# Performance work log

Hardware: AMD Instinct MI355X
Metric: run time of the kernel (lower is better)

The kernel has to match this reference:

```python
import jax, jax.numpy as jnp
import numpy as np

B, N, C = 1, 32768, 256
NH, F, AG, P = 8, 32, 64, 4  # heads, cube side, agent tokens, pool size (P**3==AG)
HD = C // NH


def setup_inputs() -> dict:
    key = jax.random.key(0)
    ks = jax.random.split(key, 4)
    s = 0.02
    return {
        "x": jax.random.normal(ks[0], (B, N, C), jnp.float32),
        "w_qkv": jax.random.normal(ks[1], (3 * C, C), jnp.float32) * s,
        "b_qkv": jnp.zeros((3 * C,), jnp.float32),
        "w_proj": jax.random.normal(ks[2], (C, C), jnp.float32) * s,
        "b_proj": jnp.zeros((C,), jnp.float32),
        "w_dwc": jax.random.normal(ks[3], (C, C, 3, 3, 3), jnp.float32) * s,
        "b_dwc": jnp.zeros((C,), jnp.float32),
    }


def reference(x, w_qkv, b_qkv, w_proj, b_proj, w_dwc, b_dwc):
    scale = HD ** -0.5
    # qkv projection -> (3, B*NH, N, HD), replicating torch reshape/permute exactly
    qkv = x @ w_qkv.T + b_qkv                       # (B, N, 3C)
    qkv = qkv.reshape(B, N, 3, NH, HD)
    qkv = jnp.transpose(qkv, (2, 0, 3, 1, 4)).reshape(3, B * NH, N, HD)
    q, k, v = qkv[0], qkv[1], qkv[2]

    # agent tokens: pool q (note torch's raw reshape interleaves heads into channels)
    q_vol = q.reshape(B, F, F, F, C)                # faithful to torch reshape
    q_vol = jnp.transpose(q_vol, (0, 4, 1, 2, 3))   # (B, C, F, F, F)
    blk = F // P
    A = q_vol.reshape(B, C, P, blk, P, blk, P, blk).mean(axis=(3, 5, 7))  # (B,C,P,P,P)
    A = A.reshape(B, C, AG).transpose(0, 2, 1)      # (B, AG, C)
    A = A.reshape(B, AG, NH, HD).transpose(0, 2, 1, 3).reshape(B * NH, AG, HD)

    # stage 1: agents attend to keys, aggregate values
    agent_attn = jax.nn.softmax((A * scale) @ jnp.swapaxes(k, -2, -1), axis=-1)  # (B*NH, AG, N)
    agent_v = agent_attn @ v                        # (B*NH, AG, HD)
    # stage 2: queries attend to agents
    q_attn = jax.nn.softmax((q * scale) @ jnp.swapaxes(A, -2, -1), axis=-1)      # (B*NH, N, AG)
    o = q_attn @ agent_v                            # (B*NH, N, HD)

    # faithful to torch: transpose(1,2) then raw reshape
    o = jnp.swapaxes(o, 1, 2).reshape(B, N, C)

    # conv residual on v: (B*NH, N, HD) -> (B, C, F, F, F)
    v5 = jnp.swapaxes(v, 1, 2).reshape(B, C, F, F, F)
    conv = jax.lax.conv_general_dilated(
        v5, w_dwc, window_strides=(1, 1, 1), padding="SAME",
        dimension_numbers=("NCDHW", "OIDHW", "NCDHW"))
    conv = conv + b_dwc[None, :, None, None, None]
    o = o + jnp.transpose(conv, (0, 2, 3, 4, 1)).reshape(B, N, C)

    return o @ w_proj.T + b_proj
```

## Files before the change

kernel.cpp:

```cpp
#include <hip/hip_runtime.h>
#include <stdint.h>

typedef unsigned short u16;
typedef __attribute__((ext_vector_type(8))) short bf16x8;
typedef __attribute__((ext_vector_type(4))) float f32x4;

#define KSCALE (0.17677669529663687f / 512.0f)

__device__ __forceinline__ u16 f2b(float f) {
  unsigned u = __float_as_uint(f);
  unsigned r = (u + 0x7fffu + ((u >> 16) & 1u)) >> 16;
  return (u16)r;
}
__device__ __forceinline__ float b2f(u16 s) { return __uint_as_float(((unsigned)s) << 16); }

__device__ __forceinline__ void async16(const void* g, void* l) {
  __builtin_amdgcn_global_load_lds((const __attribute__((address_space(1))) unsigned int*)g,
                                   (__attribute__((address_space(3))) unsigned int*)l, 16, 0, 0);
}

__device__ __forceinline__ bf16x8 frag8(const float* p, float k) {
  float4 f0 = *(const float4*)p, f1 = *(const float4*)(p + 4);
  bf16x8 v;
  v[0] = f2b(f0.x * k); v[1] = f2b(f0.y * k); v[2] = f2b(f0.z * k); v[3] = f2b(f0.w * k);
  v[4] = f2b(f1.x * k); v[5] = f2b(f1.y * k); v[6] = f2b(f1.z * k); v[7] = f2b(f1.w * k);
  return v;
}

__global__ void prep_cast(const float* __restrict__ x, const float* __restrict__ wq,
                          const float* __restrict__ wp, const float* __restrict__ wdwc,
                          u16* __restrict__ Xb, u16* __restrict__ Wqb,
                          u16* __restrict__ Wpb, u16* __restrict__ Wc) {
  int b = blockIdx.x, tid = threadIdx.x;
  if (b < 8448) {
    const float* src; u16* dst; int i;
    if (b < 8192)      { src = x;  dst = Xb;  i = b * 256 + tid; }
    else if (b < 8384) { src = wq; dst = Wqb; i = (b - 8192) * 256 + tid; }
    else               { src = wp; dst = Wpb; i = (b - 8384) * 256 + tid; }
    const float4 v = ((const float4*)src)[i];
    uint2 o;
    o.x = (unsigned)f2b(v.x) | ((unsigned)f2b(v.y) << 16);
    o.y = (unsigned)f2b(v.z) | ((unsigned)f2b(v.w) << 16);
    ((uint2*)dst)[i] = o;
  } else {
    int o = b - 8448;
    __shared__ u16 lds[6912];
    for (int t = tid; t < 6912; t += 256) lds[t] = f2b(wdwc[o * 6912 + t]);
    __syncthreads();
    for (int idx = tid; idx < 6912; idx += 256) {
      int tp = idx >> 8, i = idx & 255;
      Wc[o * 6912 + idx] = lds[i * 27 + tp];
    }
  }
}

__global__ void prep_av(const u16* __restrict__ QKV, u16* __restrict__ v5,
                        float* __restrict__ Apre) {
  int b = blockIdx.x, tid = threadIdx.x;
  if (b < 4913) {
    int idx = b * 256 + tid;
    int c8 = idx & 31, vox = idx >> 5;
    int z = vox / 1156, r2 = vox - z * 1156, y = r2 / 34, x = r2 - y * 34;
    bf16x8 val = {0, 0, 0, 0, 0, 0, 0, 0};
    if (z >= 1 && z <= 32 && y >= 1 && y <= 32 && x >= 1 && x <= 32) {
      int n = (z - 1) * 1024 + (y - 1) * 32 + (x - 1);
      val = *(const bf16x8*)(QKV + n * 768 + 512 + c8 * 8);
    }
    *(bf16x8*)(v5 + vox * 256 + c8 * 8) = val;
  } else {
    int b2 = b - 4913;
    int a = b2 >> 3, s = b2 & 7;
    int hp = tid >> 5, dp = tid & 31;
    int p1 = a >> 4, p2 = (a >> 2) & 3, p3 = a & 3;
    float sum = 0.f;
    for (int ui = 0; ui < 64; ++ui) {
      int u = s * 64 + ui;
      int f1 = p1 * 8 + (u >> 6);
      int f2 = p2 * 8 + ((u >> 3) & 7);
      int f3 = p3 * 8 + (u & 7);
      int vox = f1 * 1024 + f2 * 32 + f3;
      int n  = ((vox & 4095) << 3) + hp;
      int cq = ((vox >> 12) << 5) + dp;
      sum += b2f(QKV[n * 768 + cq]);
    }
    atomicAdd(&Apre[(hp * 64 + a) * 32 + dp], sum);
  }
}


__device__ __forceinline__ void stage64(const u16* src, int row0, int ld, int k0,
                                        short* dst, int tid) {
  int wv = tid >> 6, lane = tid & 63;
  int r15 = lane & 15, kc8 = (lane >> 4) * 8;
#pragma unroll
  for (int j = 0; j < 4; ++j) {
    int p = j & 1, g = wv * 2 + (j >> 1);
    async16(src + (row0 + g * 16 + r15) * ld + k0 + p * 32 + kc8, dst + p * 4096 + g * 512);
  }
}

__device__ __forceinline__ void mfma64(const short* As, const short* Bs, int wm, int wn,
                                       int lane, f32x4 acc[4][4]) {
  const int q = lane >> 4, c = lane & 15;
  const int fo = q * 128 + c * 8;
#pragma unroll
  for (int p = 0; p < 2; ++p) {
    bf16x8 a[4], b[4];
#pragma unroll
    for (int mt = 0; mt < 4; ++mt) a[mt] = *(const bf16x8*)&As[p * 4096 + (wm * 4 + mt) * 512 + fo];
#pragma unroll
    for (int nt = 0; nt < 4; ++nt) b[nt] = *(const bf16x8*)&Bs[p * 4096 + (wn * 4 + nt) * 512 + fo];
#pragma unroll
    for (int mt = 0; mt < 4; ++mt)
#pragma unroll
      for (int nt = 0; nt < 4; ++nt)
        acc[mt][nt] = __builtin_amdgcn_mfma_f32_16x16x32_bf16(a[mt], b[nt], acc[mt][nt], 0, 0, 0);
  }
}

__global__ __launch_bounds__(256) void gemm_qkv(const u16* __restrict__ Xb,
                                                const u16* __restrict__ Wq,
                                                const float* __restrict__ bias,
                                                u16* __restrict__ QKV) {
  const int m0 = blockIdx.x * 128, n0 = blockIdx.y * 128;
  const int tid = threadIdx.x, lane = tid & 63, wv = tid >> 6;
  const int wm = wv >> 1, wn = wv & 1, q = lane >> 4, c = lane & 15;
  __shared__ short As[8192], Bs[8192];
  f32x4 acc[4][4] = {};
  for (int kb = 0; kb < 256; kb += 64) {
    stage64(Xb, m0, 256, kb, As, tid);
    stage64(Wq, n0, 256, kb, Bs, tid);
    __syncthreads();
    mfma64(As, Bs, wm, wn, lane, acc);
    __syncthreads();
  }
#pragma unroll
  for (int nt = 0; nt < 4; ++nt) {
    int col = n0 + wn * 64 + nt * 16 + c;
    float bv = bias[col];
#pragma unroll
    for (int mt = 0; mt < 4; ++mt) {
      int row = m0 + wm * 64 + mt * 16 + q * 4;
#pragma unroll
      for (int r = 0; r < 4; ++r) QKV[(row + r) * 768 + col] = f2b(acc[mt][nt][r] + bv);
    }
  }
}

__global__ __launch_bounds__(256) void conv_s1(const u16* __restrict__ v5,
                                               const u16* __restrict__ Wc,
                                               const float* __restrict__ bias,
                                               u16* __restrict__ Xp,
                                               const u16* __restrict__ QKV,
                                               const float* __restrict__ Apre,
                                               float* __restrict__ avac,
                                               float* __restrict__ rsum) {
  extern __shared__ char smem[];
  const int tid = threadIdx.x, lane = tid & 63, wv = tid >> 6;
  const int q = lane >> 4, c = lane & 15;
  if (blockIdx.x < 512) {
    const int bid = blockIdx.x;
    const int xcd = bid & 7, idx = bid >> 3;
    const int n0 = (idx & 1) * 128;
    const int mt_i = xcd * 32 + (idx >> 1);
    const int m0 = mt_i * 128;
    const int z0 = mt_i >> 3, y0 = (mt_i & 7) * 4;
    const int wm = wv >> 1, wn = wv & 1;
    const int r15 = lane & 15, kq8 = (lane >> 4) * 8;
    short* As = (short*)smem;
    short* Bs = (short*)(smem + 9216);
    f32x4 acc[4][4] = {};
    const u16* browB = Wc + (n0 + r15) * 6912 + kq8;
    for (int dzy = 0; dzy < 9; ++dzy) {
      int dz = dzy / 3, dy = dzy - dz * 3;
      int base = (z0 + dz) * 1156 + (y0 + dy) * 34;
      int tap0 = dzy * 3;
      for (int panel = 0; panel < 8; ++panel) {
        int choff = panel * 32 + kq8;
        for (int g = wv; g < 9; g += 4) {
          int row = base + g * 16 + r15;
          row = row < 39303 ? row : 39303;
          async16(v5 + row * 256 + choff, As + g * 512);
        }
#pragma unroll
        for (int i = wv; i < 24; i += 4) {
          int dx = i >> 3, g = i & 7;
          async16(browB + g * (16 * 6912) + (tap0 + dx) * 256 + panel * 32, Bs + i * 512);
        }
        __syncthreads();
#pragma unroll
        for (int dx = 0; dx < 3; ++dx) {
          bf16x8 a[4], b[4];
#pragma unroll
          for (int mt = 0; mt < 4; ++mt) {
            int M = wm * 64 + mt * 16 + c;
            int vx = M + 2 * (M >> 5) + dx;
            a[mt] = *(const bf16x8*)&As[(vx >> 4) * 512 + q * 128 + (vx & 15) * 8];
          }
#pragma unroll
          for (int nt = 0; nt < 4; ++nt)
            b[nt] = *(const bf16x8*)&Bs[dx * 4096 + (wn * 4 + nt) * 512 + q * 128 + c * 8];
#pragma unroll
          for (int mt = 0; mt < 4; ++mt)
#pragma unroll
            for (int nt = 0; nt < 4; ++nt)
              acc[mt][nt] = __builtin_amdgcn_mfma_f32_16x16x32_bf16(a[mt], b[nt], acc[mt][nt], 0, 0, 0);
        }
        __syncthreads();
      }
    }
#pragma unroll
    for (int nt = 0; nt < 4; ++nt) {
      int col = n0 + wn * 64 + nt * 16 + c;
      float bv = bias[col];
#pragma unroll
      for (int mt = 0; mt < 4; ++mt) {
        int row = m0 + wm * 64 + mt * 16 + q * 4;
#pragma unroll
        for (int r = 0; r < 4; ++r) Xp[(row + r) * 256 + col] = f2b(acc[mt][nt][r] + bv);
      }
    }
  } else {
    const int vb = blockIdx.x - 512;
    const int h = vb >> 7, n0 = (vb & 127) * 256;
    u16* E  = (u16*)smem;
    u16* VT = (u16*)(smem + 33792);
    float* RED = (float*)smem;
    {
      const u16* vrow = QKV + (n0 + tid) * 768 + 512 + h * 32;
#pragma unroll
      for (int d8 = 0; d8 < 4; ++d8) {
        bf16x8 v = *(const bf16x8*)(vrow + d8 * 8);
#pragma unroll
        for (int e = 0; e < 8; ++e) VT[(d8 * 8 + e) * 264 + tid] = (u16)v[e];
      }
    }
    {
      bf16x8 af[4], bf[4];
#pragma unroll
      for (int mt = 0; mt < 4; ++mt)
        af[mt] = frag8(Apre + h * 2048 + (mt * 16 + c) * 32 + q * 8, KSCALE);
#pragma unroll
      for (int nt = 0; nt < 4; ++nt)
        bf[nt] = *(const bf16x8*)(QKV + (n0 + wv * 64 + nt * 16 + c) * 768 + 256 + h * 32 + q * 8);
#pragma unroll
      for (int mt = 0; mt < 4; ++mt)
#pragma unroll
        for (int nt = 0; nt < 4; ++nt) {
          f32x4 s = {0.f, 0.f, 0.f, 0.f};
          s = __builtin_amdgcn_mfma_f32_16x16x32_bf16(af[mt], bf[nt], s, 0, 0, 0);
#pragma unroll
          for (int r = 0; r < 4; ++r) {
            int a = mt * 16 + q * 4 + r, nl = wv * 64 + nt * 16 + c;
            E[a * 264 + nl] = f2b(__expf(s[r]));
          }
        }
    }
    __syncthreads();
    {
      int a = tid >> 2, seg = tid & 3;
      float sum = 0.f;
      for (int i = 0; i < 64; ++i) sum += b2f(E[a * 264 + seg * 64 + i]);
      sum += __shfl_xor(sum, 1);
      sum += __shfl_xor(sum, 2);
      if (seg == 0) atomicAdd(&rsum[h * 64 + a], sum);
    }
    f32x4 pv[4][2] = {};
#pragma unroll
    for (int ks = 0; ks < 2; ++ks) {
      bf16x8 ap[4], bp[2];
#pragma unroll
      for (int mt = 0; mt < 4; ++mt)
        ap[mt] = *(const bf16x8*)&E[(mt * 16 + c) * 264 + wv * 64 + ks * 32 + q * 8];
#pragma unroll
      for (int nt = 0; nt < 2; ++nt)
        bp[nt] = *(const bf16x8*)&VT[(nt * 16 + c) * 264 + wv * 64 + ks * 32 + q * 8];
#pragma unroll
      for (int mt = 0; mt < 4; ++mt)
#pragma unroll
        for (int nt = 0; nt < 2; ++nt)
          pv[mt][nt] = __builtin_amdgcn_mfma_f32_16x16x32_bf16(ap[mt], bp[nt], pv[mt][nt], 0, 0, 0);
    }
    __syncthreads();
#pragma unroll
    for (int mt = 0; mt < 4; ++mt)
#pragma unroll
      for (int nt = 0; nt < 2; ++nt)
#pragma unroll
        for (int r = 0; r < 4; ++r)
          RED[wv * 2048 + (mt * 16 + q * 4 + r) * 32 + nt * 16 + c] = pv[mt][nt][r];
    __syncthreads();
    for (int idx = tid; idx < 2048; idx += 256) {
      float t = RED[idx] + RED[2048 + idx] + RED[4096 + idx] + RED[6144 + idx];
      atomicAdd(&avac[h * 2048 + idx], t);
    }
  }
}

__global__ __launch_bounds__(256) void gemm_proj(const u16* __restrict__ Xp,
                                                 const u16* __restrict__ Wp,
                                                 const float* __restrict__ bias,
                                                 float* __restrict__ out) {
  const int m0 = blockIdx.x * 128, n0 = blockIdx.y * 128;
  const int tid = threadIdx.x, lane = tid & 63, wv = tid >> 6;
  const int wm = wv >> 1, wn = wv & 1, q = lane >> 4, c = lane & 15;
  __shared__ short As[8192], Bs[8192];
  f32x4 acc[4][4] = {};
  for (int kb = 0; kb < 256; kb += 64) {
    stage64(Xp, m0, 256, kb, As, tid);
    stage64(Wp, n0, 256, kb, Bs, tid);
    __syncthreads();
    mfma64(As, Bs, wm, wn, lane, acc);
    __syncthreads();
  }
#pragma unroll
  for (int nt = 0; nt < 4; ++nt) {
    int col = n0 + wn * 64 + nt * 16 + c;
    float bv = bias[col];
#pragma unroll
    for (int mt = 0; mt < 4; ++mt) {
      int row = m0 + wm * 64 + mt * 16 + q * 4;
#pragma unroll
      for (int r = 0; r < 4; ++r) out[(row + r) * 256 + col] = acc[mt][nt][r] + bv;
    }
  }
}

__global__ __launch_bounds__(256) void s2_attn(const u16* __restrict__ QKV,
                                               const float* __restrict__ Apre,
                                               const float* __restrict__ avac,
                                               const float* __restrict__ rsum,
                                               u16* __restrict__ Xp) {
  const int h = blockIdx.y, n0 = blockIdx.x * 256;
  const int tid = threadIdx.x, lane = tid & 63, wv = tid >> 6;
  const int q = lane >> 4, c = lane & 15;
  extern __shared__ char smem[];
  u16* P = (u16*)smem;
  float* O = (float*)smem;
  u16* AVT = (u16*)(smem + 36864);

  for (int j = 0; j < 8; ++j) {
    int i = j * 256 + tid;
    int a = i >> 5, d = i & 31;
    AVT[d * 72 + a] = f2b(avac[h * 2048 + i] / rsum[h * 64 + a]);
  }

  f32x4 s[4][4];
  {
    bf16x8 af[4], bf[4];
#pragma unroll
    for (int mt = 0; mt < 4; ++mt)
      af[mt] = *(const bf16x8*)(QKV + (n0 + wv * 64 + mt * 16 + c) * 768 + h * 32 + q * 8);
#pragma unroll
    for (int nt = 0; nt < 4; ++nt)
      bf[nt] = frag8(Apre + h * 2048 + (nt * 16 + c) * 32 + q * 8, KSCALE);
#pragma unroll
    for (int mt = 0; mt < 4; ++mt)
#pragma unroll
      for (int nt = 0; nt < 4; ++nt) {
        f32x4 z = {0.f, 0.f, 0.f, 0.f};
        s[mt][nt] = __builtin_amdgcn_mfma_f32_16x16x32_bf16(af[mt], bf[nt], z, 0, 0, 0);
      }
  }
#pragma unroll
  for (int mt = 0; mt < 4; ++mt)
#pragma unroll
    for (int r = 0; r < 4; ++r) {
      float v0 = s[mt][0][r], v1 = s[mt][1][r], v2 = s[mt][2][r], v3 = s[mt][3][r];
      float mx = fmaxf(fmaxf(v0, v1), fmaxf(v2, v3));
      mx = fmaxf(mx, __shfl_xor(mx, 1));
      mx = fmaxf(mx, __shfl_xor(mx, 2));
      mx = fmaxf(mx, __shfl_xor(mx, 4));
      mx = fmaxf(mx, __shfl_xor(mx, 8));
      float e0 = __expf(v0 - mx), e1 = __expf(v1 - mx), e2 = __expf(v2 - mx), e3 = __expf(v3 - mx);
      float sm = e0 + e1 + e2 + e3;
      sm += __shfl_xor(sm, 1);
      sm += __shfl_xor(sm, 2);
      sm += __shfl_xor(sm, 4);
      sm += __shfl_xor(sm, 8);
      float inv = 1.0f / sm;
      int tok = wv * 64 + mt * 16 + q * 4 + r;
      P[tok * 72 +      c] = f2b(e0 * inv);
      P[tok * 72 + 16 + c] = f2b(e1 * inv);
      P[tok * 72 + 32 + c] = f2b(e2 * inv);
      P[tok * 72 + 48 + c] = f2b(e3 * inv);
    }
  __syncthreads();
  f32x4 o[4][2] = {};
#pragma unroll
  for (int ks = 0; ks < 2; ++ks) {
    bf16x8 ap[4], bv[2];
#pragma unroll
    for (int mt = 0; mt < 4; ++mt)
      ap[mt] = *(const bf16x8*)&P[(wv * 64 + mt * 16 + c) * 72 + ks * 32 + q * 8];
#pragma unroll
    for (int nt = 0; nt < 2; ++nt)
      bv[nt] = *(const bf16x8*)&AVT[(nt * 16 + c) * 72 + ks * 32 + q * 8];
#pragma unroll
    for (int mt = 0; mt < 4; ++mt)
#pragma unroll
      for (int nt = 0; nt < 2; ++nt)
        o[mt][nt] = __builtin_amdgcn_mfma_f32_16x16x32_bf16(ap[mt], bv[nt], o[mt][nt], 0, 0, 0);
  }
  __syncthreads();
#pragma unroll
  for (int mt = 0; mt < 4; ++mt)
#pragma unroll
    for (int nt = 0; nt < 2; ++nt)
#pragma unroll
      for (int r = 0; r < 4; ++r)
        O[(nt * 16 + c) * 258 + wv * 64 + mt * 16 + q * 4 + r] = o[mt][nt][r];
  __syncthreads();
  for (int d = 0; d < 32; ++d) {
    int addr = (h * 32 + d) * 32768 + n0 + tid;
    Xp[addr] = f2b(b2f(Xp[addr]) + O[d * 258 + tid]);
  }
}


extern "C" void kernel_launch(void* const* d_in, const int* in_sizes, int n_in,
                              void* d_out, int out_size, void* d_ws, size_t ws_size,
                              hipStream_t stream) {
  const float* x      = (const float*)d_in[0];
  const float* w_qkv  = (const float*)d_in[1];
  const float* b_qkv  = (const float*)d_in[2];
  const float* w_proj = (const float*)d_in[3];
  const float* b_proj = (const float*)d_in[4];
  const float* w_dwc  = (const float*)d_in[5];
  const float* b_dwc  = (const float*)d_in[6];
  float* out = (float*)d_out;
  char* ws = (char*)d_ws;

  u16* Xb   = (u16*)(ws);
  u16* QKV  = (u16*)(ws + 16777216);
  u16* V5   = (u16*)(ws + 67108864);
  u16* Wc   = (u16*)(ws + 87232512);
  u16* Wqb  = (u16*)(ws + 90771456);
  u16* Wpb  = (u16*)(ws + 91164672);
  float* AVAC = (float*)(ws + 91361280);
  float* RSUM = (float*)(ws + 91426816);
  float* APRE = (float*)(ws + 91428864);
  u16* Xp = Xb;

  hipMemsetAsync(AVAC, 0, 65536 + 2048 + 65536, stream);
  prep_cast<<<8704, 256, 0, stream>>>(x, w_qkv, w_proj, w_dwc, Xb, Wqb, Wpb, Wc);
  gemm_qkv<<<dim3(256, 6), 256, 0, stream>>>(Xb, Wqb, b_qkv, QKV);
  prep_av<<<5425, 256, 0, stream>>>(QKV, V5, APRE);
  conv_s1<<<1536, 256, 50688, stream>>>(V5, Wc, b_dwc, Xp, QKV, APRE, AVAC, RSUM);
  s2_attn<<<dim3(128, 8), 256, 41472, stream>>>(QKV, APRE, AVAC, RSUM, Xp);
  gemm_proj<<<dim3(256, 2), 256, 0, stream>>>(Xp, Wpb, b_proj, out);
}
```

Baseline: 333.8 us.

## Halve stage-1 token tile and cut conv_s1 shared memory for higher occupancy

Stage-1 agent-attention blocks now process 128 tokens instead of 256, doubling their count to 2048. Dynamic shared memory for the fused conv/stage-1 kernel drops from 50688 to 33792 bytes, and launch bounds now request 4 blocks per CU. The cross-wave reduction is restructured into a two-phase write-then-accumulate over half the RED buffer. The goals are more resident blocks and less LDS pressure. The cost is twice as many atomicAdds into avac/rsum, and the occupancy hint may cap registers for the conv GEMM path.

```diff
diff --git a/kernel.cpp b/kernel.cpp
--- a/kernel.cpp
+++ b/kernel.cpp
@@ -147,14 +147,14 @@
   }
 }
 
-__global__ __launch_bounds__(256) void conv_s1(const u16* __restrict__ v5,
-                                               const u16* __restrict__ Wc,
-                                               const float* __restrict__ bias,
-                                               u16* __restrict__ Xp,
-                                               const u16* __restrict__ QKV,
-                                               const float* __restrict__ Apre,
-                                               float* __restrict__ avac,
-                                               float* __restrict__ rsum) {
+__global__ __launch_bounds__(256, 4) void conv_s1(const u16* __restrict__ v5,
+                                                  const u16* __restrict__ Wc,
+                                                  const float* __restrict__ bias,
+                                                  u16* __restrict__ Xp,
+                                                  const u16* __restrict__ QKV,
+                                                  const float* __restrict__ Apre,
+                                                  float* __restrict__ avac,
+                                                  float* __restrict__ rsum) {
   extern __shared__ char smem[];
   const int tid = threadIdx.x, lane = tid & 63, wv = tid >> 6;
   const int q = lane >> 4, c = lane & 15;
@@ -222,37 +222,38 @@
     }
   } else {
     const int vb = blockIdx.x - 512;
-    const int h = vb >> 7, n0 = (vb & 127) * 256;
+    const int h = vb >> 8, n0 = (vb & 255) * 128;
     u16* E  = (u16*)smem;
-    u16* VT = (u16*)(smem + 33792);
+    u16* VT = (u16*)(smem + 17408);
     float* RED = (float*)smem;
     {
-      const u16* vrow = QKV + (n0 + tid) * 768 + 512 + h * 32;
-#pragma unroll
-      for (int d8 = 0; d8 < 4; ++d8) {
+      const int tok = tid & 127, dh = (tid >> 7) * 16;
+      const u16* vrow = QKV + (n0 + tok) * 768 + 512 + h * 32 + dh;
+#pragma unroll
+      for (int d8 = 0; d8 < 2; ++d8) {
         bf16x8 v = *(const bf16x8*)(vrow + d8 * 8);
 #pragma unroll
-        for (int e = 0; e < 8; ++e) VT[(d8 * 8 + e) * 264 + tid] = (u16)v[e];
+        for (int e = 0; e < 8; ++e) VT[(dh + d8 * 8 + e) * 136 + tok] = (u16)v[e];
       }
     }
     {
-      bf16x8 af[4], bf[4];
+      bf16x8 af[4], bf[2];
 #pragma unroll
       for (int mt = 0; mt < 4; ++mt)
         af[mt] = frag8(Apre + h * 2048 + (mt * 16 + c) * 32 + q * 8, KSCALE);
 #pragma unroll
-      for (int nt = 0; nt < 4; ++nt)
-        bf[nt] = *(const bf16x8*)(QKV + (n0 + wv * 64 + nt * 16 + c) * 768 + 256 + h * 32 + q * 8);
-#pragma unroll
-      for (int mt = 0; mt < 4; ++mt)
-#pragma unroll
-        for (int nt = 0; nt < 4; ++nt) {
+      for (int nt = 0; nt < 2; ++nt)
+        bf[nt] = *(const bf16x8*)(QKV + (n0 + wv * 32 + nt * 16 + c) * 768 + 256 + h * 32 + q * 8);
+#pragma unroll
+      for (int mt = 0; mt < 4; ++mt)
+#pragma unroll
+        for (int nt = 0; nt < 2; ++nt) {
           f32x4 s = {0.f, 0.f, 0.f, 0.f};
           s = __builtin_amdgcn_mfma_f32_16x16x32_bf16(af[mt], bf[nt], s, 0, 0, 0);
 #pragma unroll
           for (int r = 0; r < 4; ++r) {
-            int a = mt * 16 + q * 4 + r, nl = wv * 64 + nt * 16 + c;
-            E[a * 264 + nl] = f2b(__expf(s[r]));
+            int a = mt * 16 + q * 4 + r, nl = wv * 32 + nt * 16 + c;
+            E[a * 136 + nl] = f2b(__expf(s[r]));
           }
         }
     }
@@ -260,21 +261,20 @@
     {
       int a = tid >> 2, seg = tid & 3;
       float sum = 0.f;
-      for (int i = 0; i < 64; ++i) sum += b2f(E[a * 264 + seg * 64 + i]);
+      for (int i = 0; i < 32; ++i) sum += b2f(E[a * 136 + seg * 32 + i]);
       sum += __shfl_xor(sum, 1);
       sum += __shfl_xor(sum, 2);
       if (seg == 0) atomicAdd(&rsum[h * 64 + a], sum);
     }
     f32x4 pv[4][2] = {};
-#pragma unroll
-    for (int ks = 0; ks < 2; ++ks) {
+    {
       bf16x8 ap[4], bp[2];
 #pragma unroll
       for (int mt = 0; mt < 4; ++mt)
-        ap[mt] = *(const bf16x8*)&E[(mt * 16 + c) * 264 + wv * 64 + ks * 32 + q * 8];
+        ap[mt] = *(const bf16x8*)&E[(mt * 16 + c) * 136 + wv * 32 + q * 8];
 #pragma unroll
       for (int nt = 0; nt < 2; ++nt)
-        bp[nt] = *(const bf16x8*)&VT[(nt * 16 + c) * 264 + wv * 64 + ks * 32 + q * 8];
+        bp[nt] = *(const bf16x8*)&VT[(nt * 16 + c) * 136 + wv * 32 + q * 8];
 #pragma unroll
       for (int mt = 0; mt < 4; ++mt)
 #pragma unroll
@@ -282,18 +282,29 @@
           pv[mt][nt] = __builtin_amdgcn_mfma_f32_16x16x32_bf16(ap[mt], bp[nt], pv[mt][nt], 0, 0, 0);
     }
     __syncthreads();
-#pragma unroll
-    for (int mt = 0; mt < 4; ++mt)
-#pragma unroll
-      for (int nt = 0; nt < 2; ++nt)
-#pragma unroll
-        for (int r = 0; r < 4; ++r)
-          RED[wv * 2048 + (mt * 16 + q * 4 + r) * 32 + nt * 16 + c] = pv[mt][nt][r];
-    __syncthreads();
-    for (int idx = tid; idx < 2048; idx += 256) {
-      float t = RED[idx] + RED[2048 + idx] + RED[4096 + idx] + RED[6144 + idx];
-      atomicAdd(&avac[h * 2048 + idx], t);
-    }
+    const int rr = wv & 1;
+    if ((wv >> 1) == 0) {
+#pragma unroll
+      for (int mt = 0; mt < 4; ++mt)
+#pragma unroll
+        for (int nt = 0; nt < 2; ++nt)
+#pragma unroll
+          for (int r = 0; r < 4; ++r)
+            RED[rr * 2048 + (mt * 16 + q * 4 + r) * 32 + nt * 16 + c] = pv[mt][nt][r];
+    }
+    __syncthreads();
+    if ((wv >> 1) == 1) {
+#pragma unroll
+      for (int mt = 0; mt < 4; ++mt)
+#pragma unroll
+        for (int nt = 0; nt < 2; ++nt)
+#pragma unroll
+          for (int r = 0; r < 4; ++r)
+            RED[rr * 2048 + (mt * 16 + q * 4 + r) * 32 + nt * 16 + c] += pv[mt][nt][r];
+    }
+    __syncthreads();
+    for (int idx = tid; idx < 2048; idx += 256)
+      atomicAdd(&avac[h * 2048 + idx], RED[idx] + RED[2048 + idx]);
   }
 }
 
@@ -446,7 +457,7 @@
   prep_cast<<<8704, 256, 0, stream>>>(x, w_qkv, w_proj, w_dwc, Xb, Wqb, Wpb, Wc);
   gemm_qkv<<<dim3(256, 6), 256, 0, stream>>>(Xb, Wqb, b_qkv, QKV);
   prep_av<<<5425, 256, 0, stream>>>(QKV, V5, APRE);
-  conv_s1<<<1536, 256, 50688, stream>>>(V5, Wc, b_dwc, Xp, QKV, APRE, AVAC, RSUM);
+  conv_s1<<<2560, 256, 33792, stream>>>(V5, Wc, b_dwc, Xp, QKV, APRE, AVAC, RSUM);
   s2_attn<<<dim3(128, 8), 256, 41472, stream>>>(QKV, APRE, AVAC, RSUM, Xp);
   gemm_proj<<<dim3(256, 2), 256, 0, stream>>>(Xp, Wpb, b_proj, out);
 }
```

Result: slower. 351.2 us (+5.2%).
